# Optimization experiments

Measured on AMD Instinct MI355X. Metric: run time of the kernel, lower is better.

The kernel has to match this reference:

```python
import jax, jax.numpy as jnp
import numpy as np

N_ENV = 100000
D_PS = 512
N_SPECIES = 4
N_SUPPORT = 256
N_STRUCT = 1000
ZETA = 2


def setup_inputs() -> dict:
    key = jax.random.key(0)
    k1, k2, k3, k4, k5 = jax.random.split(key, 5)
    power_spectrum = jax.random.normal(k1, (N_ENV, D_PS), dtype=jnp.float32)
    sp = jax.random.normal(k2, (N_SPECIES, N_SUPPORT, D_PS), dtype=jnp.float32)
    # CosineKernel asserts support points are unit-norm
    support_points = sp / jnp.linalg.norm(sp, axis=-1, keepdims=True)
    weights = jax.random.normal(k3, (N_SPECIES, 1, N_SUPPORT), dtype=jnp.float32)
    all_species = jax.random.randint(k4, (N_ENV,), 0, N_SPECIES, dtype=jnp.int64)
    structure_ids = jnp.sort(jax.random.randint(k5, (N_ENV,), 0, N_STRUCT, dtype=jnp.int64))
    return {
        "power_spectrum": power_spectrum,
        "support_points": support_points,
        "weights": weights,
        "all_species": all_species,
        "structure_ids": structure_ids,
    }


def reference(power_spectrum, support_points, weights, all_species, structure_ids):
    # Normalize each environment's power spectrum (CosineKernel)
    ps = power_spectrum / jnp.linalg.norm(power_spectrum, axis=1, keepdims=True)
    # Kernel of every environment against every species' support set: [N, S, M]
    k = jnp.einsum("nd,smd->nsm", ps, support_points) ** ZETA
    # Per-row energy contribution for each species: k @ weights[s].T -> [N, S]
    contrib = jnp.einsum("nsm,sm->ns", k, weights[:, 0, :])
    # Species masking: each row only contributes through its own species' kernel
    onehot = jax.nn.one_hot(all_species, N_SPECIES, dtype=contrib.dtype)  # [N, S]
    per_row = jnp.sum(contrib * onehot, axis=1)  # [N]
    # Segmented sum over structures (equivalent to looping over structures_slices)
    energy = jax.ops.segment_sum(per_row, structure_ids, num_segments=N_STRUCT)
    return energy[:, None]  # [n_structures, 1]
```

## Files before the change

kernel.cpp:

```cpp
#include <hip/hip_runtime.h>
#include <hip/hip_bf16.h>


constexpr int kNEnv     = 100000;
constexpr int kDPS      = 512;
constexpr int kNSpecies = 4;
constexpr int kNSupport = 256;
constexpr int kCap      = 32768;

constexpr int BN = 64;
constexpr int BK = 32;

typedef __attribute__((ext_vector_type(8))) short short8;
typedef __attribute__((ext_vector_type(4))) float f32x4;

__device__ __forceinline__ short8 pack_bf16x8(const float4& a, const float4& b) {
  union { short8 v; __hip_bfloat162 h[4]; } u;
  u.h[0] = __float22bfloat162_rn({a.x, a.y});
  u.h[1] = __float22bfloat162_rn({a.z, a.w});
  u.h[2] = __float22bfloat162_rn({b.x, b.y});
  u.h[3] = __float22bfloat162_rn({b.z, b.w});
  return u.v;
}

__device__ __forceinline__ void gload_lds16(const float* g, float* l) {
  __builtin_amdgcn_global_load_lds(
      (const __attribute__((address_space(1))) void*)g,
      (__attribute__((address_space(3))) void*)l, 16, 0, 0);
}

__global__ void scatter_convert_kernel(const float* __restrict__ sp,
                                       const int* __restrict__ species,
                                       const int* __restrict__ sid,
                                       int* __restrict__ cnt, int* __restrict__ perm,
                                       int* __restrict__ sidp, short* __restrict__ spb) {
  const int t = threadIdx.x;
  const int b = blockIdx.x;
  if (b < (kNSpecies * kNSupport * kDPS) / (256 * 8)) {
    const int base = (b * 256 + t) * 8;
    const float4 lo = *(const float4*)(sp + base);
    const float4 hi = *(const float4*)(sp + base + 4);
    *(short8*)(spb + base) = pack_bf16x8(lo, hi);
  }
  __shared__ int lcnt[kNSpecies];
  __shared__ int lbase[kNSpecies];
  if (t < kNSpecies) lcnt[t] = 0;
  __syncthreads();
  const int i = b * 256 + t;
  const bool v = i < kNEnv;
  int s = 0, r = 0, g = 0;
  if (v) { s = species[i]; r = atomicAdd(&lcnt[s], 1); g = sid[i]; }
  __syncthreads();
  if (t < kNSpecies) lbase[t] = lcnt[t] ? atomicAdd(&cnt[t], lcnt[t]) : 0;
  __syncthreads();
  if (v) {
    const int d = s * kCap + lbase[s] + r;
    perm[d] = i;
    sidp[d] = g;
  }
}

__global__ __launch_bounds__(256, 3) void gap_gemm_kernel(
    const float* __restrict__ ps, const short* __restrict__ spb,
    const float* __restrict__ w, const int* __restrict__ cnt,
    const int* __restrict__ perm, const int* __restrict__ sidp,
    float* __restrict__ energy) {
  const int s     = blockIdx.z;
  const int count = min(cnt[s], kCap);
  const int tile0 = blockIdx.x * BN;
  if (tile0 >= count) return;

  __shared__ float a_lds[2][BN * BK];
  __shared__ float red[4][BN];
  __shared__ float sqs[BN];

  const int tid  = threadIdx.x;
  const int wv   = tid >> 6;
  const int lane = tid & 63;
  const int l15  = lane & 15;
  const int lq   = lane >> 4;

  const int sby = (((lane & 7) << 4) ^ ((lane >> 3) << 4));
  const float* ssrc[2];
  #pragma unroll
  for (int c = 0; c < 2; ++c) {
    int r  = wv * 16 + c * 8 + (lane >> 3);
    int ge = tile0 + r;
    ge = ge < count ? ge : count - 1;
    ssrc[c] = ps + (size_t)perm[s * kCap + ge] * kDPS + (sby >> 2);
  }
  const int dof0 = (wv * 16) * BK;
  const int dof1 = (wv * 16 + 8) * BK;

  const short* bptr[4];
  float wgt[4];
  const float* w_s = w + s * kNSupport;
  #pragma unroll
  for (int fj = 0; fj < 4; ++fj) {
    const int m = wv * 64 + fj * 16 + l15;
    bptr[fj] = spb + ((size_t)s * kNSupport + m) * kDPS + lq * 8;
    wgt[fj]  = w_s[m];
  }

  const int fswz = (l15 & 7) << 4;
  const int cb1  = (lq * 32) ^ fswz;
  const int cb2  = (lq * 32 + 16) ^ fswz;
  const int rowb = l15 * 128;

  f32x4 acc[4][4];
  #pragma unroll
  for (int fi = 0; fi < 4; ++fi)
    #pragma unroll
    for (int fj = 0; fj < 4; ++fj) acc[fi][fj] = (f32x4)0.f;
  float sq[4] = {0.f, 0.f, 0.f, 0.f};

#define STAGE(BUF, K0) do {                        \
    gload_lds16(ssrc[0] + (K0), &a_lds[BUF][dof0]); \
    gload_lds16(ssrc[1] + (K0), &a_lds[BUF][dof1]); \
  } while (0)

#define BODY(BUF, K0) do {                                                      \
    short8 bf[4];                                                               \
    _Pragma("unroll")                                                           \
    for (int fj = 0; fj < 4; ++fj) bf[fj] = *(const short8*)(bptr[fj] + (K0));  \
    const char* abase = (const char*)&a_lds[BUF][0];                            \
    _Pragma("unroll")                                                           \
    for (int fi = 0; fi < 4; ++fi) {                                            \
      const float4 f1 = *(const float4*)(abase + fi * 2048 + rowb + cb1);       \
      const float4 f2 = *(const float4*)(abase + fi * 2048 + rowb + cb2);       \
      if (wv == 0)                                                              \
        sq[fi] += f1.x * f1.x + f1.y * f1.y + f1.z * f1.z + f1.w * f1.w         \
                + f2.x * f2.x + f2.y * f2.y + f2.z * f2.z + f2.w * f2.w;        \
      const short8 af = pack_bf16x8(f1, f2);                                    \
      _Pragma("unroll")                                                         \
      for (int fj = 0; fj < 4; ++fj)                                            \
        acc[fi][fj] =                                                           \
            __builtin_amdgcn_mfma_f32_16x16x32_bf16(af, bf[fj], acc[fi][fj], 0, 0, 0); \
    }                                                                           \
  } while (0)

  STAGE(0, 0);
  __syncthreads();

  #pragma unroll 1
  for (int kp = 0; kp < kDPS; kp += 2 * BK) {
    STAGE(1, kp + BK);
    BODY(0, kp);
    __syncthreads();
    if (kp + 2 * BK < kDPS) STAGE(0, kp + 2 * BK);
    BODY(1, kp + BK);
    __syncthreads();
  }

#undef STAGE
#undef BODY

  if (wv == 0) {
    #pragma unroll
    for (int fi = 0; fi < 4; ++fi) {
      float p = sq[fi];
      p += __shfl_xor(p, 16, 64);
      p += __shfl_xor(p, 32, 64);
      if (lane < 16) sqs[fi * 16 + lane] = p;
    }
  }

  #pragma unroll
  for (int fi = 0; fi < 4; ++fi) {
    #pragma unroll
    for (int r = 0; r < 4; ++r) {
      float p = 0.f;
      #pragma unroll
      for (int fj = 0; fj < 4; ++fj) {
        const float c = acc[fi][fj][r];
        p += c * c * wgt[fj];
      }
      p += __shfl_xor(p, 1, 64);
      p += __shfl_xor(p, 2, 64);
      p += __shfl_xor(p, 4, 64);
      p += __shfl_xor(p, 8, 64);
      if (l15 == 0) red[wv][fi * 16 + lq * 4 + r] = p;
    }
  }
  __syncthreads();
  if (tid < BN) {
    const float v = red[0][tid] + red[1][tid] + red[2][tid] + red[3][tid];
    const int g  = tile0 + tid;
    if (g < count) atomicAdd(&energy[sidp[s * kCap + g]], v / sqs[tid]);
  }
}

extern "C" void kernel_launch(void* const* d_in, const int* in_sizes, int n_in,
                              void* d_out, int out_size, void* d_ws, size_t ws_size,
                              hipStream_t stream) {
  const float* ps      = (const float*)d_in[0];
  const float* sp      = (const float*)d_in[1];
  const float* w       = (const float*)d_in[2];
  const int*   species = (const int*)d_in[3];
  const int*   sid     = (const int*)d_in[4];
  float* energy = (float*)d_out;

  char* wsb  = (char*)d_ws;
  int*   cnt  = (int*)wsb;
  int*   perm = (int*)(wsb + 256);
  int*   sidp = (int*)(wsb + 256 + 4 * kCap * sizeof(int));
  short* spb  = (short*)(wsb + 256 + 8 * kCap * sizeof(int));

  hipMemsetAsync(cnt, 0, 16, stream);
  hipMemsetAsync(energy, 0, out_size * sizeof(float), stream);

  scatter_convert_kernel<<<(kNEnv + 255) / 256, 256, 0, stream>>>(
      sp, species, sid, cnt, perm, sidp, spb);

  dim3 grid(kCap / BN, 1, kNSpecies);
  gap_gemm_kernel<<<grid, 256, 0, stream>>>(ps, spb, w, cnt, perm, sidp, energy);
}
```

Measured before the change: 347.0 us.

## Precompute bf16 rows and inverse norms, deepen GEMM pipeline with manual waitcnt

A new pre-pass kernel converts every power-spectrum row to bf16 and stores its inverse squared norm. The GEMM kernel then streams bf16 rows into a 4-deep LDS ring, using raw s_barrier and explicit vmcnt waits in a fully unrolled K loop, and applies the stored inverse norm in the epilogue. This removes the per-tile fp32-to-bf16 packing, the norm accumulation and half the A-tile bytes in the main loop. In exchange it adds an extra full pass over the input and a bf16 workspace copy. The scatter kernel also switches from LDS atomics to wave ballots, and the old path is kept as a fallback when the workspace is too small.

```diff
diff --git a/kernel.cpp b/kernel.cpp
--- a/kernel.cpp
+++ b/kernel.cpp
@@ -23,7 +23,7 @@
   return u.v;
 }
 
-__device__ __forceinline__ void gload_lds16(const float* g, float* l) {
+__device__ __forceinline__ void gload_lds16(const void* g, void* l) {
   __builtin_amdgcn_global_load_lds(
       (const __attribute__((address_space(1))) void*)g,
       (__attribute__((address_space(3))) void*)l, 16, 0, 0);
@@ -42,37 +42,71 @@
     const float4 hi = *(const float4*)(sp + base + 4);
     *(short8*)(spb + base) = pack_bf16x8(lo, hi);
   }
-  __shared__ int lcnt[kNSpecies];
-  __shared__ int lbase[kNSpecies];
-  if (t < kNSpecies) lcnt[t] = 0;
-  __syncthreads();
-  const int i = b * 256 + t;
-  const bool v = i < kNEnv;
-  int s = 0, r = 0, g = 0;
-  if (v) { s = species[i]; r = atomicAdd(&lcnt[s], 1); g = sid[i]; }
-  __syncthreads();
-  if (t < kNSpecies) lbase[t] = lcnt[t] ? atomicAdd(&cnt[t], lcnt[t]) : 0;
+  const int wv   = t >> 6;
+  const int lane = t & 63;
+  const int i    = b * 256 + t;
+  const bool v   = i < kNEnv;
+  int s = -1, g = 0;
+  if (v) { s = species[i]; g = sid[i]; }
+
+  unsigned long long m[kNSpecies];
+  #pragma unroll
+  for (int k = 0; k < kNSpecies; ++k) m[k] = __ballot(s == k);
+  int r = 0;
+  if (v) r = __popcll(m[s] & ((1ull << lane) - 1ull));
+
+  __shared__ int wcnt[4][kNSpecies];
+  __shared__ int wbase[4][kNSpecies];
+  if (lane < kNSpecies) wcnt[wv][lane] = (int)__popcll(m[lane]);
+  __syncthreads();
+  if (t < kNSpecies) {
+    const int k = t;
+    const int tot = wcnt[0][k] + wcnt[1][k] + wcnt[2][k] + wcnt[3][k];
+    int p = tot ? atomicAdd(&cnt[k], tot) : 0;
+    #pragma unroll
+    for (int wvi = 0; wvi < 4; ++wvi) { wbase[wvi][k] = p; p += wcnt[wvi][k]; }
+  }
   __syncthreads();
   if (v) {
-    const int d = s * kCap + lbase[s] + r;
+    const int d = s * kCap + wbase[wv][s] + r;
     perm[d] = i;
     sidp[d] = g;
   }
 }
 
-__global__ __launch_bounds__(256, 3) void gap_gemm_kernel(
-    const float* __restrict__ ps, const short* __restrict__ spb,
-    const float* __restrict__ w, const int* __restrict__ cnt,
-    const int* __restrict__ perm, const int* __restrict__ sidp,
-    float* __restrict__ energy) {
+__global__ __launch_bounds__(256) void norm_convert_kernel(
+    const float* __restrict__ ps, short* __restrict__ psb, float* __restrict__ invn) {
+  const int wv   = threadIdx.x >> 6;
+  const int lane = threadIdx.x & 63;
+  const int row  = blockIdx.x * 4 + wv;
+  if (row >= kNEnv) return;
+  const float* src = ps + (size_t)row * kDPS + lane * 8;
+  const float4 a = *(const float4*)(src);
+  const float4 b = *(const float4*)(src + 4);
+  float sq = a.x * a.x + a.y * a.y + a.z * a.z + a.w * a.w
+           + b.x * b.x + b.y * b.y + b.z * b.z + b.w * b.w;
+  sq += __shfl_xor(sq, 1, 64);
+  sq += __shfl_xor(sq, 2, 64);
+  sq += __shfl_xor(sq, 4, 64);
+  sq += __shfl_xor(sq, 8, 64);
+  sq += __shfl_xor(sq, 16, 64);
+  sq += __shfl_xor(sq, 32, 64);
+  *(short8*)(psb + (size_t)row * kDPS + lane * 8) = pack_bf16x8(a, b);
+  if (lane == 0) invn[row] = 1.0f / sq;
+}
+
+__global__ __launch_bounds__(256, 3) void gap_gemm_v6(
+    const short* __restrict__ psb, const short* __restrict__ spb,
+    const float* __restrict__ w, const float* __restrict__ invn,
+    const int* __restrict__ cnt, const int* __restrict__ perm,
+    const int* __restrict__ sidp, float* __restrict__ energy) {
   const int s     = blockIdx.z;
   const int count = min(cnt[s], kCap);
   const int tile0 = blockIdx.x * BN;
   if (tile0 >= count) return;
 
-  __shared__ float a_lds[2][BN * BK];
+  __shared__ short a_lds[4][BN * BK];
   __shared__ float red[4][BN];
-  __shared__ float sqs[BN];
 
   const int tid  = threadIdx.x;
   const int wv   = tid >> 6;
@@ -80,17 +114,12 @@
   const int l15  = lane & 15;
   const int lq   = lane >> 4;
 
-  const int sby = (((lane & 7) << 4) ^ ((lane >> 3) << 4));
-  const float* ssrc[2];
-  #pragma unroll
-  for (int c = 0; c < 2; ++c) {
-    int r  = wv * 16 + c * 8 + (lane >> 3);
-    int ge = tile0 + r;
-    ge = ge < count ? ge : count - 1;
-    ssrc[c] = ps + (size_t)perm[s * kCap + ge] * kDPS + (sby >> 2);
-  }
-  const int dof0 = (wv * 16) * BK;
-  const int dof1 = (wv * 16 + 8) * BK;
+  {
+  }
+  const int srow = wv * 16 + (lane >> 2);
+  int ge = tile0 + srow;
+  ge = ge < count ? ge : count - 1;
+  const short* s_src = psb + (size_t)perm[s * kCap + ge] * kDPS + (lane & 3) * 8;
 
   const short* bptr[4];
   float wgt[4];
@@ -102,68 +131,66 @@
     wgt[fj]  = w_s[m];
   }
 
-  const int fswz = (l15 & 7) << 4;
-  const int cb1  = (lq * 32) ^ fswz;
-  const int cb2  = (lq * 32 + 16) ^ fswz;
-  const int rowb = l15 * 128;
-
   f32x4 acc[4][4];
   #pragma unroll
   for (int fi = 0; fi < 4; ++fi)
     #pragma unroll
     for (int fj = 0; fj < 4; ++fj) acc[fi][fj] = (f32x4)0.f;
-  float sq[4] = {0.f, 0.f, 0.f, 0.f};
-
-#define STAGE(BUF, K0) do {                        \
-    gload_lds16(ssrc[0] + (K0), &a_lds[BUF][dof0]); \
-    gload_lds16(ssrc[1] + (K0), &a_lds[BUF][dof1]); \
-  } while (0)
-
-#define BODY(BUF, K0) do {                                                      \
-    short8 bf[4];                                                               \
-    _Pragma("unroll")                                                           \
-    for (int fj = 0; fj < 4; ++fj) bf[fj] = *(const short8*)(bptr[fj] + (K0));  \
-    const char* abase = (const char*)&a_lds[BUF][0];                            \
-    _Pragma("unroll")                                                           \
-    for (int fi = 0; fi < 4; ++fi) {                                            \
-      const float4 f1 = *(const float4*)(abase + fi * 2048 + rowb + cb1);       \
-      const float4 f2 = *(const float4*)(abase + fi * 2048 + rowb + cb2);       \
-      if (wv == 0)                                                              \
-        sq[fi] += f1.x * f1.x + f1.y * f1.y + f1.z * f1.z + f1.w * f1.w         \
-                + f2.x * f2.x + f2.y * f2.y + f2.z * f2.z + f2.w * f2.w;        \
-      const short8 af = pack_bf16x8(f1, f2);                                    \
-      _Pragma("unroll")                                                         \
-      for (int fj = 0; fj < 4; ++fj)                                            \
-        acc[fi][fj] =                                                           \
-            __builtin_amdgcn_mfma_f32_16x16x32_bf16(af, bf[fj], acc[fi][fj], 0, 0, 0); \
-    }                                                                           \
-  } while (0)
-
-  STAGE(0, 0);
-  __syncthreads();
-
-  #pragma unroll 1
-  for (int kp = 0; kp < kDPS; kp += 2 * BK) {
-    STAGE(1, kp + BK);
-    BODY(0, kp);
-    __syncthreads();
-    if (kp + 2 * BK < kDPS) STAGE(0, kp + 2 * BK);
-    BODY(1, kp + BK);
-    __syncthreads();
-  }
-
-#undef STAGE
-#undef BODY
-
-  if (wv == 0) {
-    #pragma unroll
-    for (int fi = 0; fi < 4; ++fi) {
-      float p = sq[fi];
-      p += __shfl_xor(p, 16, 64);
-      p += __shfl_xor(p, 32, 64);
-      if (lane < 16) sqs[fi * 16 + lane] = p;
-    }
-  }
+
+  short8 bf0[4], bf1[4];
+
+#define STAGEV6(T) gload_lds16(s_src + (T) * BK, &a_lds[(T) & 3][wv * 512])
+#define BLOADV6(T, BF) do {                                            \
+    _Pragma("unroll")                                                  \
+    for (int fj = 0; fj < 4; ++fj)                                     \
+      BF[fj] = *(const short8*)(bptr[fj] + (T) * BK);                  \
+  } while (0)
+#define BODYV6(T, BF) do {                                             \
+    short8 af[4];                                                      \
+    _Pragma("unroll")                                                  \
+    for (int fi = 0; fi < 4; ++fi)                                     \
+      af[fi] = *(const short8*)&a_lds[(T) & 3][fi * 512 + l15 * 32 + lq * 8]; \
+    _Pragma("unroll")                                                  \
+    for (int fi = 0; fi < 4; ++fi)                                     \
+      _Pragma("unroll")                                                \
+      for (int fj = 0; fj < 4; ++fj)                                   \
+        acc[fi][fj] = __builtin_amdgcn_mfma_f32_16x16x32_bf16(         \
+            af[fi], BF[fj], acc[fi][fj], 0, 0, 0);                     \
+  } while (0)
+
+#define STEPV6(T, VN, BFCUR, BFNXT) do {                               \
+    asm volatile("s_barrier" ::: "memory");                            \
+    if ((T) + 1 < 16) BLOADV6((T) + 1, BFNXT);                         \
+    if ((T) + 2 < 16) STAGEV6((T) + 2);                                \
+    asm volatile("s_waitcnt vmcnt(" #VN ")" ::: "memory");             \
+    BODYV6(T, BFCUR);                                                  \
+  } while (0)
+
+  STAGEV6(0);
+  STAGEV6(1);
+  BLOADV6(0, bf0);
+
+  STEPV6(0,  10, bf0, bf1);
+  STEPV6(1,  10, bf1, bf0);
+  STEPV6(2,  10, bf0, bf1);
+  STEPV6(3,  10, bf1, bf0);
+  STEPV6(4,  10, bf0, bf1);
+  STEPV6(5,  10, bf1, bf0);
+  STEPV6(6,  10, bf0, bf1);
+  STEPV6(7,  10, bf1, bf0);
+  STEPV6(8,  10, bf0, bf1);
+  STEPV6(9,  10, bf1, bf0);
+  STEPV6(10, 10, bf0, bf1);
+  STEPV6(11, 10, bf1, bf0);
+  STEPV6(12, 10, bf0, bf1);
+  STEPV6(13, 10, bf1, bf0);
+  STEPV6(14,  9, bf0, bf1);
+  STEPV6(15,  4, bf1, bf0);
+
+#undef STEPV6
+#undef BODYV6
+#undef BLOADV6
+#undef STAGEV6
 
   #pragma unroll
   for (int fi = 0; fi < 4; ++fi) {
@@ -186,6 +213,138 @@
   if (tid < BN) {
     const float v = red[0][tid] + red[1][tid] + red[2][tid] + red[3][tid];
     const int g  = tile0 + tid;
+    if (g < count) {
+      const int arow = perm[s * kCap + g];
+      atomicAdd(&energy[sidp[s * kCap + g]], v * invn[arow]);
+    }
+  }
+}
+
+__global__ __launch_bounds__(256, 3) void gap_gemm_v5(
+    const float* __restrict__ ps, const short* __restrict__ spb,
+    const float* __restrict__ w, const int* __restrict__ cnt,
+    const int* __restrict__ perm, const int* __restrict__ sidp,
+    float* __restrict__ energy) {
+  const int s     = blockIdx.z;
+  const int count = min(cnt[s], kCap);
+  const int tile0 = blockIdx.x * BN;
+  if (tile0 >= count) return;
+
+  __shared__ float a_lds[2][BN * BK];
+  __shared__ float red[4][BN];
+  __shared__ float sqs[BN];
+
+  const int tid  = threadIdx.x;
+  const int wv   = tid >> 6;
+  const int lane = tid & 63;
+  const int l15  = lane & 15;
+  const int lq   = lane >> 4;
+
+  const int sby = (((lane & 7) << 4) ^ ((lane >> 3) << 4));
+  const float* ssrc[2];
+  #pragma unroll
+  for (int c = 0; c < 2; ++c) {
+    int r  = wv * 16 + c * 8 + (lane >> 3);
+    int ge = tile0 + r;
+    ge = ge < count ? ge : count - 1;
+    ssrc[c] = ps + (size_t)perm[s * kCap + ge] * kDPS + (sby >> 2);
+  }
+  const int dof0 = (wv * 16) * BK;
+  const int dof1 = (wv * 16 + 8) * BK;
+
+  const short* bptr[4];
+  float wgt[4];
+  const float* w_s = w + s * kNSupport;
+  #pragma unroll
+  for (int fj = 0; fj < 4; ++fj) {
+    const int m = wv * 64 + fj * 16 + l15;
+    bptr[fj] = spb + ((size_t)s * kNSupport + m) * kDPS + lq * 8;
+    wgt[fj]  = w_s[m];
+  }
+
+  const int fswz = (l15 & 7) << 4;
+  const int cb1  = (lq * 32) ^ fswz;
+  const int cb2  = (lq * 32 + 16) ^ fswz;
+  const int rowb = l15 * 128;
+
+  f32x4 acc[4][4];
+  #pragma unroll
+  for (int fi = 0; fi < 4; ++fi)
+    #pragma unroll
+    for (int fj = 0; fj < 4; ++fj) acc[fi][fj] = (f32x4)0.f;
+  float sq[4] = {0.f, 0.f, 0.f, 0.f};
+
+#define STAGE5(BUF, K0) do {                                   \
+    gload_lds16(ssrc[0] + (K0), &a_lds[BUF][dof0]);            \
+    gload_lds16(ssrc[1] + (K0), &a_lds[BUF][dof1]);            \
+  } while (0)
+#define BODY5(BUF, K0) do {                                                     \
+    short8 bfv[4];                                                              \
+    _Pragma("unroll")                                                           \
+    for (int fj = 0; fj < 4; ++fj) bfv[fj] = *(const short8*)(bptr[fj] + (K0)); \
+    const char* abase = (const char*)&a_lds[BUF][0];                            \
+    _Pragma("unroll")                                                           \
+    for (int fi = 0; fi < 4; ++fi) {                                            \
+      const float4 f1 = *(const float4*)(abase + fi * 2048 + rowb + cb1);       \
+      const float4 f2 = *(const float4*)(abase + fi * 2048 + rowb + cb2);       \
+      if (wv == 0)                                                              \
+        sq[fi] += f1.x * f1.x + f1.y * f1.y + f1.z * f1.z + f1.w * f1.w         \
+                + f2.x * f2.x + f2.y * f2.y + f2.z * f2.z + f2.w * f2.w;        \
+      const short8 af = pack_bf16x8(f1, f2);                                    \
+      _Pragma("unroll")                                                         \
+      for (int fj = 0; fj < 4; ++fj)                                            \
+        acc[fi][fj] =                                                           \
+            __builtin_amdgcn_mfma_f32_16x16x32_bf16(af, bfv[fj], acc[fi][fj], 0, 0, 0); \
+    }                                                                           \
+  } while (0)
+
+  STAGE5(0, 0);
+  __syncthreads();
+
+  #pragma unroll 1
+  for (int kp = 0; kp < kDPS; kp += 2 * BK) {
+    STAGE5(1, kp + BK);
+    BODY5(0, kp);
+    __syncthreads();
+    if (kp + 2 * BK < kDPS) STAGE5(0, kp + 2 * BK);
+    BODY5(1, kp + BK);
+    __syncthreads();
+  }
+
+#undef STAGE5
+#undef BODY5
+
+  if (wv == 0) {
+    #pragma unroll
+    for (int fi = 0; fi < 4; ++fi) {
+      float p = sq[fi];
+      p += __shfl_xor(p, 16, 64);
+      p += __shfl_xor(p, 32, 64);
+      if (lane < 16) sqs[fi * 16 + lane] = p;
+    }
+  }
+
+  #pragma unroll
+  for (int fi = 0; fi < 4; ++fi) {
+    #pragma unroll
+    for (int r = 0; r < 4; ++r) {
+      float p = 0.f;
+      #pragma unroll
+      for (int fj = 0; fj < 4; ++fj) {
+        const float c = acc[fi][fj][r];
+        p += c * c * wgt[fj];
+      }
+      p += __shfl_xor(p, 1, 64);
+      p += __shfl_xor(p, 2, 64);
+      p += __shfl_xor(p, 4, 64);
+      p += __shfl_xor(p, 8, 64);
+      if (l15 == 0) red[wv][fi * 16 + lq * 4 + r] = p;
+    }
+  }
+  __syncthreads();
+  if (tid < BN) {
+    const float v = red[0][tid] + red[1][tid] + red[2][tid] + red[3][tid];
+    const int g  = tile0 + tid;
     if (g < count) atomicAdd(&energy[sidp[s * kCap + g]], v / sqs[tid]);
   }
 }
@@ -200,11 +359,20 @@
   const int*   sid     = (const int*)d_in[4];
   float* energy = (float*)d_out;
 
-  char* wsb  = (char*)d_ws;
+  char* wsb = (char*)d_ws;
+  constexpr size_t kOffPerm = 256;
+  constexpr size_t kOffSidp = kOffPerm + (size_t)kNSpecies * kCap * 4;
+  constexpr size_t kOffSpb  = kOffSidp + (size_t)kNSpecies * kCap * 4;
+  constexpr size_t kOffInvn = kOffSpb + (size_t)kNSpecies * kNSupport * kDPS * 2;
+  constexpr size_t kOffPsb  = (kOffInvn + (size_t)kNEnv * 4 + 255) & ~(size_t)255;
+  constexpr size_t kWsNeed  = kOffPsb + (size_t)kNEnv * kDPS * 2;
+
   int*   cnt  = (int*)wsb;
-  int*   perm = (int*)(wsb + 256);
-  int*   sidp = (int*)(wsb + 256 + 4 * kCap * sizeof(int));
-  short* spb  = (short*)(wsb + 256 + 8 * kCap * sizeof(int));
+  int*   perm = (int*)(wsb + kOffPerm);
+  int*   sidp = (int*)(wsb + kOffSidp);
+  short* spb  = (short*)(wsb + kOffSpb);
+  float* invn = (float*)(wsb + kOffInvn);
+  short* psb  = (short*)(wsb + kOffPsb);
 
   hipMemsetAsync(cnt, 0, 16, stream);
   hipMemsetAsync(energy, 0, out_size * sizeof(float), stream);
@@ -212,6 +380,12 @@
   scatter_convert_kernel<<<(kNEnv + 255) / 256, 256, 0, stream>>>(
       sp, species, sid, cnt, perm, sidp, spb);
 
-  dim3 grid(kCap / BN, 1, kNSpecies);
-  gap_gemm_kernel<<<grid, 256, 0, stream>>>(ps, spb, w, cnt, perm, sidp, energy);
-}
+  if (ws_size >= kWsNeed) {
+    norm_convert_kernel<<<(kNEnv + 3) / 4, 256, 0, stream>>>(ps, psb, invn);
+    dim3 grid(kCap / BN, 1, kNSpecies);
+    gap_gemm_v6<<<grid, 256, 0, stream>>>(psb, spb, w, invn, cnt, perm, sidp, energy);
+  } else {
+    dim3 grid(kCap / BN, 1, kNSpecies);
+    gap_gemm_v5<<<grid, 256, 0, stream>>>(ps, spb, w, cnt, perm, sidp, energy);
+  }
+}
```

After: 391.0 us. +12.7%, slower.

## Deepen GEMM pipeline to 4 LDS stages and compact scatter via ballot

Applied to the files above, without the earlier changes.

The GEMM main loop is fully unrolled into 16 steps. It uses a 4-deep LDS ring for the A tiles, prefetches two tiles ahead, and double-buffers the B fragments in registers. Explicit vmcnt waits replace the paired __syncthreads, and s_setprio raises priority around the MFMA bodies, so more load latency is hidden behind compute. The scatter kernel swaps shared-memory atomics for wave ballots and popcounts, which adds per-wave offsets. The extra LDS for four buffers may lower occupancy, and the hand-counted vmcnt values must stay in step with the issued loads.

```diff
diff --git a/kernel.cpp b/kernel.cpp
--- a/kernel.cpp
+++ b/kernel.cpp
@@ -23,7 +23,7 @@
   return u.v;
 }
 
-__device__ __forceinline__ void gload_lds16(const float* g, float* l) {
+__device__ __forceinline__ void gload_lds16(const void* g, void* l) {
   __builtin_amdgcn_global_load_lds(
       (const __attribute__((address_space(1))) void*)g,
       (__attribute__((address_space(3))) void*)l, 16, 0, 0);
@@ -42,25 +42,39 @@
     const float4 hi = *(const float4*)(sp + base + 4);
     *(short8*)(spb + base) = pack_bf16x8(lo, hi);
   }
-  __shared__ int lcnt[kNSpecies];
-  __shared__ int lbase[kNSpecies];
-  if (t < kNSpecies) lcnt[t] = 0;
+  const int wv   = t >> 6;
+  const int lane = t & 63;
+  const int i    = b * 256 + t;
+  const bool v   = i < kNEnv;
+  int s = -1, g = 0;
+  if (v) { s = species[i]; g = sid[i]; }
+
+  unsigned long long m[kNSpecies];
+  #pragma unroll
+  for (int k = 0; k < kNSpecies; ++k) m[k] = __ballot(s == k);
+  int r = 0;
+  if (v) r = __popcll(m[s] & ((1ull << lane) - 1ull));
+
+  __shared__ int wcnt[4][kNSpecies];
+  __shared__ int wbase[4][kNSpecies];
+  if (lane < kNSpecies) wcnt[wv][lane] = (int)__popcll(m[lane]);
   __syncthreads();
-  const int i = b * 256 + t;
-  const bool v = i < kNEnv;
-  int s = 0, r = 0, g = 0;
-  if (v) { s = species[i]; r = atomicAdd(&lcnt[s], 1); g = sid[i]; }
-  __syncthreads();
-  if (t < kNSpecies) lbase[t] = lcnt[t] ? atomicAdd(&cnt[t], lcnt[t]) : 0;
+  if (t < kNSpecies) {
+    const int k = t;
+    const int tot = wcnt[0][k] + wcnt[1][k] + wcnt[2][k] + wcnt[3][k];
+    int p = tot ? atomicAdd(&cnt[k], tot) : 0;
+    #pragma unroll
+    for (int wvi = 0; wvi < 4; ++wvi) { wbase[wvi][k] = p; p += wcnt[wvi][k]; }
+  }
   __syncthreads();
   if (v) {
-    const int d = s * kCap + lbase[s] + r;
+    const int d = s * kCap + wbase[wv][s] + r;
     perm[d] = i;
     sidp[d] = g;
   }
 }
 
-__global__ __launch_bounds__(256, 3) void gap_gemm_kernel(
+__global__ __launch_bounds__(256, 3) void gap_gemm_v7(
     const float* __restrict__ ps, const short* __restrict__ spb,
     const float* __restrict__ w, const int* __restrict__ cnt,
     const int* __restrict__ perm, const int* __restrict__ sidp,
@@ -70,7 +84,7 @@
   const int tile0 = blockIdx.x * BN;
   if (tile0 >= count) return;
 
-  __shared__ float a_lds[2][BN * BK];
+  __shared__ float a_lds[4][BN * BK];
   __shared__ float red[4][BN];
   __shared__ float sqs[BN];
 
@@ -80,7 +94,7 @@
   const int l15  = lane & 15;
   const int lq   = lane >> 4;
 
-  const int sby = (((lane & 7) << 4) ^ ((lane >> 3) << 4));
+  const int sby = ((lane & 7) << 4) ^ (((lane >> 3) & 7) << 4);
   const float* ssrc[2];
   #pragma unroll
   for (int c = 0; c < 2; ++c) {
@@ -114,16 +128,20 @@
     for (int fj = 0; fj < 4; ++fj) acc[fi][fj] = (f32x4)0.f;
   float sq[4] = {0.f, 0.f, 0.f, 0.f};
 
-#define STAGE(BUF, K0) do {                        \
-    gload_lds16(ssrc[0] + (K0), &a_lds[BUF][dof0]); \
-    gload_lds16(ssrc[1] + (K0), &a_lds[BUF][dof1]); \
-  } while (0)
-
-#define BODY(BUF, K0) do {                                                      \
-    short8 bf[4];                                                               \
-    _Pragma("unroll")                                                           \
-    for (int fj = 0; fj < 4; ++fj) bf[fj] = *(const short8*)(bptr[fj] + (K0));  \
-    const char* abase = (const char*)&a_lds[BUF][0];                            \
+  short8 bf0[4], bf1[4];
+
+#define STAGE7(T) do {                                                  \
+    gload_lds16(ssrc[0] + (T) * BK, &a_lds[(T) & 3][dof0]);             \
+    gload_lds16(ssrc[1] + (T) * BK, &a_lds[(T) & 3][dof1]);             \
+  } while (0)
+#define BLOAD7(T, BF) do {                                              \
+    _Pragma("unroll")                                                   \
+    for (int fj = 0; fj < 4; ++fj)                                      \
+      BF[fj] = *(const short8*)(bptr[fj] + (T) * BK);                   \
+  } while (0)
+#define BODY7(T, BF) do {                                                       \
+    const char* abase = (const char*)&a_lds[(T) & 3][0];                        \
+    __builtin_amdgcn_s_setprio(1);                                              \
     _Pragma("unroll")                                                           \
     for (int fi = 0; fi < 4; ++fi) {                                            \
       const float4 f1 = *(const float4*)(abase + fi * 2048 + rowb + cb1);       \
@@ -134,26 +152,45 @@
       const short8 af = pack_bf16x8(f1, f2);                                    \
       _Pragma("unroll")                                                         \
       for (int fj = 0; fj < 4; ++fj)                                            \
-        acc[fi][fj] =                                                           \
-            __builtin_amdgcn_mfma_f32_16x16x32_bf16(af, bf[fj], acc[fi][fj], 0, 0, 0); \
+        acc[fi][fj] = __builtin_amdgcn_mfma_f32_16x16x32_bf16(                  \
+            af, BF[fj], acc[fi][fj], 0, 0, 0);                                  \
     }                                                                           \
-  } while (0)
-
-  STAGE(0, 0);
-  __syncthreads();
-
-  #pragma unroll 1
-  for (int kp = 0; kp < kDPS; kp += 2 * BK) {
-    STAGE(1, kp + BK);
-    BODY(0, kp);
-    __syncthreads();
-    if (kp + 2 * BK < kDPS) STAGE(0, kp + 2 * BK);
-    BODY(1, kp + BK);
-    __syncthreads();
-  }
-
-#undef STAGE
-#undef BODY
+    __builtin_amdgcn_s_setprio(0);                                              \
+  } while (0)
+
+#define STEP7(T, VN, BFCUR, BFNXT) do {                                 \
+    if ((T) + 1 < 16) BLOAD7((T) + 1, BFNXT);                           \
+    if ((T) + 2 < 16) STAGE7((T) + 2);                                  \
+    asm volatile("s_waitcnt vmcnt(" #VN ")" ::: "memory");              \
+    __builtin_amdgcn_s_barrier();                                       \
+    BODY7(T, BFCUR);                                                    \
+  } while (0)
+
+  STAGE7(0);
+  STAGE7(1);
+  BLOAD7(0, bf0);
+
+  STEP7(0,  6, bf0, bf1);
+  STEP7(1,  8, bf1, bf0);
+  STEP7(2,  8, bf0, bf1);
+  STEP7(3,  8, bf1, bf0);
+  STEP7(4,  8, bf0, bf1);
+  STEP7(5,  8, bf1, bf0);
+  STEP7(6,  8, bf0, bf1);
+  STEP7(7,  8, bf1, bf0);
+  STEP7(8,  8, bf0, bf1);
+  STEP7(9,  8, bf1, bf0);
+  STEP7(10, 8, bf0, bf1);
+  STEP7(11, 8, bf1, bf0);
+  STEP7(12, 8, bf0, bf1);
+  STEP7(13, 8, bf1, bf0);
+  STEP7(14, 6, bf0, bf1);
+  STEP7(15, 0, bf1, bf0);
+
+#undef STEP7
+#undef BODY7
+#undef BLOAD7
+#undef STAGE7
 
   if (wv == 0) {
     #pragma unroll
@@ -200,11 +237,15 @@
   const int*   sid     = (const int*)d_in[4];
   float* energy = (float*)d_out;
 
-  char* wsb  = (char*)d_ws;
+  char* wsb = (char*)d_ws;
+  constexpr size_t kOffPerm = 256;
+  constexpr size_t kOffSidp = kOffPerm + (size_t)kNSpecies * kCap * 4;
+  constexpr size_t kOffSpb  = kOffSidp + (size_t)kNSpecies * kCap * 4;
+
   int*   cnt  = (int*)wsb;
-  int*   perm = (int*)(wsb + 256);
-  int*   sidp = (int*)(wsb + 256 + 4 * kCap * sizeof(int));
-  short* spb  = (short*)(wsb + 256 + 8 * kCap * sizeof(int));
+  int*   perm = (int*)(wsb + kOffPerm);
+  int*   sidp = (int*)(wsb + kOffSidp);
+  short* spb  = (short*)(wsb + kOffSpb);
 
   hipMemsetAsync(cnt, 0, 16, stream);
   hipMemsetAsync(energy, 0, out_size * sizeof(float), stream);
@@ -213,5 +254,5 @@
       sp, species, sid, cnt, perm, sidp, spb);
 
   dim3 grid(kCap / BN, 1, kNSpecies);
-  gap_gemm_kernel<<<grid, 256, 0, stream>>>(ps, spb, w, cnt, perm, sidp, energy);
-}
+  gap_gemm_v7<<<grid, 256, 0, stream>>>(ps, spb, w, cnt, perm, sidp, energy);
+}
```

After: 348.2 us. No clear change (+0.3%).
